# Kernel optimization log

Measured on AMD Instinct MI355X. Metric: run time of the kernel, lower is better.

## Reference

```python
import jax, jax.numpy as jnp
import numpy as np

B, N, F_IN = 32, 512, 64
HEADS = (8, 8)
HIDS = (64, 64)
EDGE_P = 0.05  # graph density
NEG_SLOPE = 0.2
NEG_INF = -1e20


def setup_inputs() -> dict:
    key = jax.random.key(0)
    ks = jax.random.split(key, 8)
    x = jax.random.normal(ks[0], (B, N, F_IN), dtype=jnp.float32)
    adj = (jax.random.uniform(ks[1], (B, N, N)) < EDGE_P).astype(jnp.float32)
    adj = jnp.maximum(adj, adj.transpose(0, 2, 1))  # symmetric adjacency
    # mask = (batch, row): every (b, n) pair gets the masked softmax
    b_idx = jnp.repeat(jnp.arange(B, dtype=jnp.int32), N)   # [B*N]
    r_idx = jnp.tile(jnp.arange(N, dtype=jnp.int32), B)     # [B*N]
    # layer 0: f_in=64 -> f_out=64, H=8 ; layer 1: f_in=64*8=512 -> f_out=64, H=8
    W0 = jax.random.normal(ks[2], (F_IN, HIDS[0]), dtype=jnp.float32) / jnp.sqrt(jnp.float32(F_IN))
    a_src0 = jax.random.normal(ks[3], (HIDS[0], HEADS[0]), dtype=jnp.float32) / jnp.sqrt(jnp.float32(HIDS[0]))
    a_dst0 = jax.random.normal(ks[4], (HIDS[0], HEADS[0]), dtype=jnp.float32) / jnp.sqrt(jnp.float32(HIDS[0]))
    f_in1 = HIDS[0] * HEADS[0]
    W1 = jax.random.normal(ks[5], (f_in1, HIDS[1]), dtype=jnp.float32) / jnp.sqrt(jnp.float32(f_in1))
    a_src1 = jax.random.normal(ks[6], (HIDS[1], HEADS[1]), dtype=jnp.float32) / jnp.sqrt(jnp.float32(HIDS[1]))
    a_dst1 = jax.random.normal(ks[7], (HIDS[1], HEADS[1]), dtype=jnp.float32) / jnp.sqrt(jnp.float32(HIDS[1]))
    return dict(x=x, adj=adj, b_idx=b_idx, r_idx=r_idx,
                W0=W0, a_src0=a_src0, a_dst0=a_dst0,
                W1=W1, a_src1=a_src1, a_dst1=a_dst1)


def _gat_layer(x, adj, b_idx, r_idx, W, a_src, a_dst):
    # x: [B,N,f_in], adj: [B,N,N] (diag already set), W: [f_in,F], a_*: [F,H]
    hp = x @ W                                        # [B,N,F]
    s = jnp.einsum('bnf,fh->bhn', hp, a_src)          # attn_src
    d = jnp.einsum('bnf,fh->bhn', hp, a_dst)          # attn_dst
    attn = s[:, :, :, None] + d[:, :, None, :]        # [B,H,N,N]
    attn = jnp.where(attn >= 0, attn, NEG_SLOPE * attn)  # leaky_relu(0.2)
    attn = jnp.where(adj[:, None, :, :] == 0, 0.0, attn)  # masked_fill(adj==0, 0)
    rows = attn[b_idx, :, r_idx, :]                   # [K,H,N]
    rows = jnp.where(rows == 0.0, NEG_INF, rows)
    rows = jax.nn.softmax(rows, axis=-1)
    attn = attn.at[b_idx, :, r_idx, :].set(rows)
    return jnp.einsum('bhij,bjf->bhif', attn, hp)     # [B,H,N,F]


def reference(x, adj, b_idx, r_idx, W0, a_src0, a_dst0, W1, a_src1, a_dst1):
    Bn, Nn = x.shape[:2]
    # torch mutates adj in place: adj[batch,row,row] = 1 (self loops)
    adj = adj.at[b_idx, r_idx, r_idx].set(1.0)
    o = _gat_layer(x, adj, b_idx, r_idx, W0, a_src0, a_dst0)      # [B,H,N,F0]
    x1 = jax.nn.elu(o.transpose(0, 2, 1, 3).reshape(Bn, Nn, -1))  # [B,N,H*F0]
    o2 = _gat_layer(x1, adj, b_idx, r_idx, W1, a_src1, a_dst1)    # [B,H,N,F1]
    return o2.mean(axis=1)                                        # [B,N,F1]
```

## Files before the change

kernel.cpp:

```cpp
#include <hip/hip_runtime.h>
#include <hip/hip_bf16.h>
#include <math.h>

#define BB 32
#define NN 512

typedef _Float16 f16x8 __attribute__((ext_vector_type(8)));
typedef float f32x4 __attribute__((ext_vector_type(4)));

#define MFMA16(a, b, c) __builtin_amdgcn_mfma_f32_16x16x32_f16(a, b, c, 0, 0, 0)

__global__ __launch_bounds__(256) void k_wt_prep(
    const float* __restrict__ W0, _Float16* __restrict__ W0T,
    const float* __restrict__ W1, _Float16* __restrict__ W1T)
{
    int id = blockIdx.x * 256 + threadIdx.x;
    const float* W; _Float16* WT; int KT, task;
    if (id < 512) { W = W0; WT = W0T; KT = 64;  task = id; }
    else          { W = W1; WT = W1T; KT = 512; task = id - 512; }
    int n = task & 63, gabs = task >> 6;
    int c = gabs >> 3, g = gabs & 7;
    f16x8 hv;
#pragma unroll
    for (int e = 0; e < 8; ++e)
        hv[e] = (_Float16)W[(size_t)(gabs * 8 + e) * 64 + n];
    *(f16x8*)(WT + (size_t)n * KT + c * 64 + (g ^ (n & 7)) * 8) = hv;
}

__global__ __launch_bounds__(256) void k_maxd(
    const float* __restrict__ dTg, float* __restrict__ maxd)
{
    __shared__ float sm[4];
    int bh = blockIdx.x;
    int t = threadIdx.x, lane = t & 63, w = t >> 6;
    const float* p = dTg + (size_t)bh * NN;
    float m = fmaxf(p[t], p[t + 256]);
#pragma unroll
    for (int off = 32; off; off >>= 1) m = fmaxf(m, __shfl_xor(m, off));
    if (lane == 0) sm[w] = m;
    __syncthreads();
    if (t == 0) maxd[bh] = fmaxf(fmaxf(sm[0], sm[1]), fmaxf(sm[2], sm[3]));
}

static __device__ __forceinline__ void epi_sd_hpt(
    const float* ctile, const float* asd_f, int row0, int t,
    float* __restrict__ s, float* __restrict__ dTg, _Float16* __restrict__ hpT)
{
    int b = row0 >> 9, jb = row0 & 511;
    if (t < 128) {
        int rr = t >> 3, h = t & 7;
        float sv = 0.f, dv = 0.f;
#pragma unroll
        for (int f = 0; f < 64; ++f) {
            float hv = ctile[rr * 66 + f];
            sv = fmaf(hv, asd_f[f * 8 + h], sv);
            dv = fmaf(hv, asd_f[512 + f * 8 + h], dv);
        }
        s[((size_t)b * NN + jb + rr) * 8 + h] = sv;
        dTg[((size_t)b * 8 + h) * NN + jb + rr] = dv;
    } else {
        int t2 = t - 128;
        int f = t2 >> 1, jl = (t2 & 1) * 8;
        f16x8 hv;
#pragma unroll
        for (int e = 0; e < 8; ++e)
            hv[e] = (_Float16)ctile[(jl + e) * 66 + f];
        *(f16x8*)(hpT + ((size_t)b * 64 + f) * NN + jb + jl) = hv;
    }
}

__global__ __launch_bounds__(256) void k_gemm0(
    const float* __restrict__ x, const _Float16* __restrict__ W0T,
    const float* __restrict__ a_src, const float* __restrict__ a_dst,
    float* __restrict__ s, float* __restrict__ dTg, _Float16* __restrict__ hpT)
{
    __shared__ float ctile[16 * 66];
    __shared__ float asd_f[1024];
    int t = threadIdx.x, row0 = blockIdx.x * 16;
    int lane = t & 63, w = t >> 6, cn = lane & 15, rq = lane >> 4;

    ((float4*)asd_f)[t] = (t < 128) ? ((const float4*)a_src)[t]
                                    : ((const float4*)a_dst)[t - 128];
    f32x4 acc;
#pragma unroll
    for (int e = 0; e < 4; ++e) acc[e] = 0.f;
#pragma unroll
    for (int ks = 0; ks < 2; ++ks) {
        const float* xp = x + (size_t)(row0 + cn) * 64 + ks * 32 + rq * 8;
        float4 x0 = *(const float4*)xp, x1 = *(const float4*)(xp + 4);
        f16x8 ah = {(_Float16)x0.x, (_Float16)x0.y, (_Float16)x0.z, (_Float16)x0.w,
                    (_Float16)x1.x, (_Float16)x1.y, (_Float16)x1.z, (_Float16)x1.w};
        int nn = w * 16 + cn;
        f16x8 bh = *(const f16x8*)(W0T + (size_t)nn * 64 + (((ks * 4 + rq) ^ (nn & 7)) * 8));
        acc = MFMA16(ah, bh, acc);
    }
#pragma unroll
    for (int r = 0; r < 4; ++r)
        ctile[(rq * 4 + r) * 66 + w * 16 + cn] = acc[r];
    __syncthreads();
    epi_sd_hpt(ctile, asd_f, row0, t, s, dTg, hpT);
}

template<int MODE>
__global__ __launch_bounds__(256, 4) void k_attn_fused(
    const float* __restrict__ adj, const float* __restrict__ s,
    const float* __restrict__ dTg, const float* __restrict__ maxd,
    const _Float16* __restrict__ hpT,
    const _Float16* __restrict__ W1T,
    const float* __restrict__ a_src, const float* __restrict__ a_dst,
    float* __restrict__ s_out, float* __restrict__ dTg_out,
    _Float16* __restrict__ hpT_out, float* __restrict__ o_f)
{
    __shared__ __align__(16) char smem[32768];
    _Float16* hT = (_Float16*)smem;

    int blk = blockIdx.x;
    int vb = ((blk & 7) << 7) | (blk >> 3);
    int b = vb >> 5, i0 = (vb & 31) << 4;
    int row0 = vb * 16;
    int t = threadIdx.x, lane = t & 63, w = t >> 6;
    int cn = lane & 15, rq = lane >> 4;
    int h0 = 2 * w, h1 = h0 + 1;
    int myrow = i0 + cn;

    float sv0 = s[((size_t)b * NN + myrow) * 8 + h0];
    float sv1 = s[((size_t)b * NN + myrow) * 8 + h1];
    float M0 = fmaxf(sv0 + maxd[b * 8 + h0], 0.f);
    float M1 = fmaxf(sv1 + maxd[b * 8 + h1], 0.f);

    const float* arow = adj + ((size_t)b * NN + myrow) * NN;
    const float* dg0 = dTg + ((size_t)b * 8 + h0) * NN;
    const float* dg1 = dTg + ((size_t)b * 8 + h1) * NN;
    const _Float16* hb = hpT + (size_t)b * 64 * NN;

    f16x8 ones;
#pragma unroll
    for (int e = 0; e < 8; ++e) ones[e] = (_Float16)1.0f;

    f32x4 acc[2][4], accrs[2];
#pragma unroll
    for (int hh = 0; hh < 2; ++hh) {
#pragma unroll
        for (int e = 0; e < 4; ++e) accrs[hh][e] = 0.f;
#pragma unroll
        for (int ft = 0; ft < 4; ++ft)
#pragma unroll
            for (int e = 0; e < 4; ++e) acc[hh][ft][e] = 0.f;
    }

    for (int jc = 0; jc < NN; jc += 64) {
#pragma unroll
        for (int u = 0; u < 2; ++u) {
            int idx = t + u * 256;
            int f = idx >> 3, g = idx & 7;
            *(uint4*)&hT[f * 64 + ((g ^ (f & 7)) * 8)] =
                *(const uint4*)(hb + (size_t)f * 512 + jc + g * 8);
        }
        __syncthreads();

        float aa[2][8], dd0[2][8], dd1[2][8];
#pragma unroll
        for (int ks = 0; ks < 2; ++ks) {
            int j0 = jc + ks * 32 + rq * 8;
            *(float4*)&aa[ks][0]  = *(const float4*)(arow + j0);
            *(float4*)&aa[ks][4]  = *(const float4*)(arow + j0 + 4);
            *(float4*)&dd0[ks][0] = *(const float4*)(dg0 + j0);
            *(float4*)&dd0[ks][4] = *(const float4*)(dg0 + j0 + 4);
            *(float4*)&dd1[ks][0] = *(const float4*)(dg1 + j0);
            *(float4*)&dd1[ks][4] = *(const float4*)(dg1 + j0 + 4);
        }
#pragma unroll
        for (int ks = 0; ks < 2; ++ks) {
            int j0 = jc + ks * 32 + rq * 8;
            int rel = myrow - j0;
            f16x8 aA, aB;
#pragma unroll
            for (int e = 0; e < 8; ++e) {
                bool con = (aa[ks][e] != 0.f) || (e == rel);
                float e0 = sv0 + dd0[ks][e];
                float l0 = fmaxf(e0, 0.2f * e0);
                float p0 = __expf(l0 - M0);
                p0 = (con && l0 != 0.f) ? p0 : 0.f;
                float e1 = sv1 + dd1[ks][e];
                float l1 = fmaxf(e1, 0.2f * e1);
                float p1 = __expf(l1 - M1);
                p1 = (con && l1 != 0.f) ? p1 : 0.f;
                aA[e] = (_Float16)p0;
                aB[e] = (_Float16)p1;
            }
            accrs[0] = MFMA16(aA, ones, accrs[0]);
            accrs[1] = MFMA16(aB, ones, accrs[1]);
#pragma unroll
            for (int ft = 0; ft < 4; ++ft) {
                int f = ft * 16 + cn;
                f16x8 bh = *(const f16x8*)&hT[f * 64 + (((ks * 4 + rq) ^ (f & 7)) * 8)];
                acc[0][ft] = MFMA16(aA, bh, acc[0][ft]);
                acc[1][ft] = MFMA16(aB, bh, acc[1][ft]);
            }
        }
        __syncthreads();
    }

    float invr[2][4];
#pragma unroll
    for (int hh = 0; hh < 2; ++hh)
#pragma unroll
        for (int r = 0; r < 4; ++r) invr[hh][r] = 1.0f / accrs[hh][r];

    if (MODE == 0) {
        _Float16* x1all = (_Float16*)(smem + 8192);
#pragma unroll
        for (int hh = 0; hh < 2; ++hh) {
            int h = h0 + hh;
#pragma unroll
            for (int ft = 0; ft < 4; ++ft)
#pragma unroll
                for (int r = 0; r < 4; ++r) {
                    int il = rq * 4 + r;
                    float v = acc[hh][ft][r] * invr[hh][r];
                    v = v > 0.f ? v : __expf(v) - 1.f;
                    int f = ft * 16 + cn;
                    x1all[h * 1024 + il * 64 + (((f >> 3) ^ (il & 7)) * 8) + (f & 7)] =
                        (_Float16)v;
                }
        }

        _Float16* Bst[2] = { (_Float16*)smem, (_Float16*)(smem + 24576) };
        {
            __syncthreads();
#pragma unroll
            for (int u = 0; u < 2; ++u) {
                int idx = t + u * 256;
                *(uint4*)&Bst[0][idx * 8] =
                    *(const uint4*)(W1T + (size_t)(idx >> 3) * 512 + (idx & 7) * 8);
            }
        }
        f32x4 g1;
#pragma unroll
        for (int e = 0; e < 4; ++e) g1[e] = 0.f;
        for (int kc = 0; kc < 8; ++kc) {
            int cur = kc & 1;
            __syncthreads();
            if (kc < 7) {
#pragma unroll
                for (int u = 0; u < 2; ++u) {
                    int idx = t + u * 256;
                    *(uint4*)&Bst[cur ^ 1][idx * 8] =
                        *(const uint4*)(W1T + (size_t)(idx >> 3) * 512 + (kc + 1) * 64 + (idx & 7) * 8);
                }
            }
#pragma unroll
            for (int ks = 0; ks < 2; ++ks) {
                int pa = (((ks * 4 + rq) ^ (cn & 7)) * 8);
                f16x8 ah = *(const f16x8*)&x1all[kc * 1024 + cn * 64 + pa];
                int nn = w * 16 + cn;
                f16x8 bh = *(const f16x8*)&Bst[cur][nn * 64 + (((ks * 4 + rq) ^ (nn & 7)) * 8)];
                g1 = MFMA16(ah, bh, g1);
            }
        }
        __syncthreads();
        float* ctile = (float*)(smem + 8192);
        float* asd_f = (float*)(smem + 16384);
#pragma unroll
        for (int r = 0; r < 4; ++r)
            ctile[(rq * 4 + r) * 66 + w * 16 + cn] = g1[r];
        ((float4*)asd_f)[t] = (t < 128) ? ((const float4*)a_src)[t]
                                        : ((const float4*)a_dst)[t - 128];
        __syncthreads();
        epi_sd_hpt(ctile, asd_f, row0, t, s_out, dTg_out, hpT_out);
    } else {
        float* red = (float*)smem;
#pragma unroll
        for (int ft = 0; ft < 4; ++ft)
#pragma unroll
            for (int r = 0; r < 4; ++r) {
                int il = rq * 4 + r;
                float v = acc[0][ft][r] * invr[0][r]
                        + acc[1][ft][r] * invr[1][r];
                red[(w * 16 + il) * 64 + ft * 16 + cn] = v;
            }
        __syncthreads();
#pragma unroll
        for (int u = 0; u < 4; ++u) {
            int idx = t + u * 256;
            int il = idx >> 6, f = idx & 63;
            float sum = red[il * 64 + f] + red[(16 + il) * 64 + f]
                      + red[(32 + il) * 64 + f] + red[(48 + il) * 64 + f];
            o_f[((size_t)b * NN + i0 + il) * 64 + f] = sum * 0.125f;
        }
    }
}

extern "C" void kernel_launch(void* const* d_in, const int* in_sizes, int n_in,
                              void* d_out, int out_size, void* d_ws, size_t ws_size,
                              hipStream_t stream) {
    const float* x      = (const float*)d_in[0];
    const float* adj    = (const float*)d_in[1];
    const float* W0     = (const float*)d_in[4];
    const float* a_src0 = (const float*)d_in[5];
    const float* a_dst0 = (const float*)d_in[6];
    const float* W1     = (const float*)d_in[7];
    const float* a_src1 = (const float*)d_in[8];
    const float* a_dst1 = (const float*)d_in[9];
    float* out = (float*)d_out;

    float* ws = (float*)d_ws;
    const size_t R = (size_t)BB * NN;
    float* s0    = ws;
    float* dTg0  = s0 + R * 8;
    float* s1    = dTg0 + (size_t)BB * 8 * NN;
    float* dTg1  = s1 + R * 8;
    float* maxd0 = dTg1 + (size_t)BB * 8 * NN;
    float* maxd1 = maxd0 + 256;
    _Float16* hp0T = (_Float16*)(maxd1 + 256);
    _Float16* hp1T = hp0T + (size_t)BB * 64 * NN;
    _Float16* W0T  = hp1T + (size_t)BB * 64 * NN;
    _Float16* W1T  = W0T + (size_t)64 * 64;

    k_wt_prep<<<18, 256, 0, stream>>>(W0, W0T, W1, W1T);
    k_gemm0<<<1024, 256, 0, stream>>>(x, W0T, a_src0, a_dst0, s0, dTg0, hp0T);
    k_maxd<<<256, 256, 0, stream>>>(dTg0, maxd0);
    k_attn_fused<0><<<1024, 256, 0, stream>>>(adj, s0, dTg0, maxd0, hp0T,
                                              W1T, a_src1, a_dst1,
                                              s1, dTg1, hp1T, nullptr);
    k_maxd<<<256, 256, 0, stream>>>(dTg1, maxd1);
    k_attn_fused<1><<<1024, 256, 0, stream>>>(adj, s1, dTg1, maxd1, hp1T,
                                              nullptr, nullptr, nullptr,
                                              nullptr, nullptr, nullptr, out);
}
```

Measured before the change: 174.6 us.

## Prefetch hp tiles and W1 chunks into registers, pack probabilities with cvt_pkrtz

The attention loop now loads the next hp^T tile into registers while the current tile is consumed, then writes it to LDS at the start of the next iteration. Previously the tile went global→LDS synchronously before each compute step. The W1 staging loop in layer-0 mode also prefetches into registers and stores to the other LDS buffer after the MFMAs, and one barrier is dropped. Probability conversion to fp16 now uses the packed round-toward-zero convert instead of per-element casts, which changes rounding slightly and adds register pressure from the prefetch buffers.

```diff
diff --git a/kernel.cpp b/kernel.cpp
--- a/kernel.cpp
+++ b/kernel.cpp
@@ -6,9 +6,12 @@
 #define NN 512
 
 typedef _Float16 f16x8 __attribute__((ext_vector_type(8)));
+typedef __fp16  fp16x2 __attribute__((ext_vector_type(2)));
 typedef float f32x4 __attribute__((ext_vector_type(4)));
 
 #define MFMA16(a, b, c) __builtin_amdgcn_mfma_f32_16x16x32_f16(a, b, c, 0, 0, 0)
+
+union AF { f16x8 v; unsigned int u[4]; };
 
 __global__ __launch_bounds__(256) void k_wt_prep(
     const float* __restrict__ W0, _Float16* __restrict__ W0T,
@@ -133,6 +136,11 @@
     const float* dg1 = dTg + ((size_t)b * 8 + h1) * NN;
     const _Float16* hb = hpT + (size_t)b * 64 * NN;
 
+    int f0 = t >> 3, g0 = t & 7;
+    int f1 = f0 + 32;
+    int sw = ((g0 ^ (f0 & 7)) * 8);
+    int sw0 = f0 * 64 + sw, sw1 = f1 * 64 + sw;
+
     f16x8 ones;
 #pragma unroll
     for (int e = 0; e < 8; ++e) ones[e] = (_Float16)1.0f;
@@ -148,16 +156,11 @@
             for (int e = 0; e < 4; ++e) acc[hh][ft][e] = 0.f;
     }
 
-    for (int jc = 0; jc < NN; jc += 64) {
-#pragma unroll
-        for (int u = 0; u < 2; ++u) {
-            int idx = t + u * 256;
-            int f = idx >> 3, g = idx & 7;
-            *(uint4*)&hT[f * 64 + ((g ^ (f & 7)) * 8)] =
-                *(const uint4*)(hb + (size_t)f * 512 + jc + g * 8);
-        }
-        __syncthreads();
-
+    uint4 rH0 = *(const uint4*)(hb + (size_t)f0 * 512 + g0 * 8);
+    uint4 rH1 = *(const uint4*)(hb + (size_t)f1 * 512 + g0 * 8);
+
+    for (int jcx = 0; jcx < 8; ++jcx) {
+        int jc = jcx * 64;
         float aa[2][8], dd0[2][8], dd1[2][8];
 #pragma unroll
         for (int ks = 0; ks < 2; ++ks) {
@@ -169,33 +172,47 @@
             *(float4*)&dd1[ks][0] = *(const float4*)(dg1 + j0);
             *(float4*)&dd1[ks][4] = *(const float4*)(dg1 + j0 + 4);
         }
+        *(uint4*)&hT[sw0] = rH0;
+        *(uint4*)&hT[sw1] = rH1;
+        __syncthreads();
+        if (jcx < 7) {
+            rH0 = *(const uint4*)(hb + (size_t)f0 * 512 + jc + 64 + g0 * 8);
+            rH1 = *(const uint4*)(hb + (size_t)f1 * 512 + jc + 64 + g0 * 8);
+        }
 #pragma unroll
         for (int ks = 0; ks < 2; ++ks) {
             int j0 = jc + ks * 32 + rq * 8;
             int rel = myrow - j0;
-            f16x8 aA, aB;
-#pragma unroll
-            for (int e = 0; e < 8; ++e) {
-                bool con = (aa[ks][e] != 0.f) || (e == rel);
-                float e0 = sv0 + dd0[ks][e];
-                float l0 = fmaxf(e0, 0.2f * e0);
-                float p0 = __expf(l0 - M0);
-                p0 = (con && l0 != 0.f) ? p0 : 0.f;
-                float e1 = sv1 + dd1[ks][e];
-                float l1 = fmaxf(e1, 0.2f * e1);
-                float p1 = __expf(l1 - M1);
-                p1 = (con && l1 != 0.f) ? p1 : 0.f;
-                aA[e] = (_Float16)p0;
-                aB[e] = (_Float16)p1;
-            }
-            accrs[0] = MFMA16(aA, ones, accrs[0]);
-            accrs[1] = MFMA16(aB, ones, accrs[1]);
+            AF aA, aB;
+#pragma unroll
+            for (int e = 0; e < 8; e += 2) {
+                float pA[2], pB[2];
+#pragma unroll
+                for (int q = 0; q < 2; ++q) {
+                    int ee = e + q;
+                    bool con = (aa[ks][ee] != 0.f) || (ee == rel);
+                    float e0 = sv0 + dd0[ks][ee];
+                    float l0 = fmaxf(e0, 0.2f * e0);
+                    float p0 = __expf(l0 - M0);
+                    pA[q] = (con && l0 != 0.f) ? p0 : 0.f;
+                    float e1 = sv1 + dd1[ks][ee];
+                    float l1 = fmaxf(e1, 0.2f * e1);
+                    float p1 = __expf(l1 - M1);
+                    pB[q] = (con && l1 != 0.f) ? p1 : 0.f;
+                }
+                fp16x2 ka = __builtin_amdgcn_cvt_pkrtz(pA[0], pA[1]);
+                fp16x2 kb = __builtin_amdgcn_cvt_pkrtz(pB[0], pB[1]);
+                aA.u[e >> 1] = __builtin_bit_cast(unsigned int, ka);
+                aB.u[e >> 1] = __builtin_bit_cast(unsigned int, kb);
+            }
+            accrs[0] = MFMA16(aA.v, ones, accrs[0]);
+            accrs[1] = MFMA16(aB.v, ones, accrs[1]);
 #pragma unroll
             for (int ft = 0; ft < 4; ++ft) {
                 int f = ft * 16 + cn;
                 f16x8 bh = *(const f16x8*)&hT[f * 64 + (((ks * 4 + rq) ^ (f & 7)) * 8)];
-                acc[0][ft] = MFMA16(aA, bh, acc[0][ft]);
-                acc[1][ft] = MFMA16(aB, bh, acc[1][ft]);
+                acc[0][ft] = MFMA16(aA.v, bh, acc[0][ft]);
+                acc[1][ft] = MFMA16(aB.v, bh, acc[1][ft]);
             }
         }
         __syncthreads();
@@ -227,7 +244,6 @@
 
         _Float16* Bst[2] = { (_Float16*)smem, (_Float16*)(smem + 24576) };
         {
-            __syncthreads();
 #pragma unroll
             for (int u = 0; u < 2; ++u) {
                 int idx = t + u * 256;
@@ -238,17 +254,14 @@
         f32x4 g1;
 #pragma unroll
         for (int e = 0; e < 4; ++e) g1[e] = 0.f;
+        uint4 rB0, rB1;
         for (int kc = 0; kc < 8; ++kc) {
             int cur = kc & 1;
+            if (kc < 7) {
+                rB0 = *(const uint4*)(W1T + (size_t)(t >> 3) * 512 + (kc + 1) * 64 + (t & 7) * 8);
+                rB1 = *(const uint4*)(W1T + (size_t)((t + 256) >> 3) * 512 + (kc + 1) * 64 + (t & 7) * 8);
+            }
             __syncthreads();
-            if (kc < 7) {
-#pragma unroll
-                for (int u = 0; u < 2; ++u) {
-                    int idx = t + u * 256;
-                    *(uint4*)&Bst[cur ^ 1][idx * 8] =
-                        *(const uint4*)(W1T + (size_t)(idx >> 3) * 512 + (kc + 1) * 64 + (idx & 7) * 8);
-                }
-            }
 #pragma unroll
             for (int ks = 0; ks < 2; ++ks) {
                 int pa = (((ks * 4 + rq) ^ (cn & 7)) * 8);
@@ -256,6 +269,10 @@
                 int nn = w * 16 + cn;
                 f16x8 bh = *(const f16x8*)&Bst[cur][nn * 64 + (((ks * 4 + rq) ^ (nn & 7)) * 8)];
                 g1 = MFMA16(ah, bh, g1);
+            }
+            if (kc < 7) {
+                *(uint4*)&Bst[cur ^ 1][t * 8] = rB0;
+                *(uint4*)&Bst[cur ^ 1][(t + 256) * 8] = rB1;
             }
         }
         __syncthreads();
```

After: 165.1 us. 5.4% less time.
